# Optimization experiments

Measured on AMD Instinct MI355X. Metric: run time of the kernel, lower is better.

## Reference

```python
import jax, jax.numpy as jnp
import numpy as np

B, I, H = 65536, 256, 256

def setup_inputs() -> dict:
    key = jax.random.key(0)
    ks = jax.random.split(key, 7)
    stdv = 1.0 / np.sqrt(H)
    u = lambda k, shape: jax.random.uniform(k, shape, jnp.float32, -stdv, stdv)
    return {
        "x":  jax.random.normal(ks[0], (B, I), jnp.float32),
        "h":  jax.random.normal(ks[1], (B, H), jnp.float32),
        "c":  jax.random.normal(ks[2], (B, H), jnp.float32),
        "Wi": u(ks[3], (4, H, I)),   # stacked [W_ii, W_if, W_ig, W_io], torch layout [out,in]
        "Wh": u(ks[4], (4, H, H)),   # stacked [W_hi, W_hf, W_hg, W_ho]
        "bi": u(ks[5], (4, H)),
        "bh": u(ks[6], (4, H)),
    }

def reference(x, h, c, Wi, Wh, bi, bh):
    # Fused version of 8 separate Linears: two batched GEMMs + one elementwise pass.
    # gates[b, k, h] = x @ Wi[k].T + h_prev @ Wh[k].T + bi[k] + bh[k]
    gates = (jnp.einsum('bi,khi->bkh', x, Wi)
             + jnp.einsum('bj,khj->bkh', h, Wh)
             + bi[None] + bh[None])
    i = jax.nn.sigmoid(gates[:, 0])
    f = jax.nn.sigmoid(gates[:, 1])
    g = jnp.tanh(gates[:, 2])
    o = jax.nn.sigmoid(gates[:, 3])
    c_new = f * c + i * g
    h_new = o * jnp.tanh(c_new)
    return (h_new, c_new)
```

## Files before the change

kernel.cpp:

```cpp
#include <hip/hip_runtime.h>
#include <stdint.h>

#define B_DIM 65536
#define HOFF  16777216

typedef __attribute__((ext_vector_type(8))) short short8;
typedef __attribute__((ext_vector_type(8))) unsigned short ushort8_t;
typedef __attribute__((ext_vector_type(4))) float f32x4;

__device__ __forceinline__ unsigned short f2bf(float f) {
  unsigned int u = __builtin_bit_cast(unsigned int, f);
  u += 0x7FFFu + ((u >> 16) & 1u);
  return (unsigned short)(u >> 16);
}
__device__ __forceinline__ float sigf(float x) { return 1.0f / (1.0f + __expf(-x)); }
__device__ __forceinline__ float tanh_fast(float x) {
  float a = fabsf(x);
  float e = __expf(-2.0f * a);
  float t = (1.0f - e) / (1.0f + e);
  return x < 0.0f ? -t : t;
}

typedef const __attribute__((address_space(1))) unsigned int* as1p;
typedef __attribute__((address_space(3))) unsigned int* as3p;
__device__ __forceinline__ void llds16(const unsigned short* g, unsigned short* l) {
  __builtin_amdgcn_global_load_lds((as1p)g, (as3p)l, 16, 0, 0);
}

__global__ void prep_a(const float* __restrict__ x, const float* __restrict__ h,
                       ushort8_t* __restrict__ A8) {
  unsigned o = blockIdx.x * 256u + threadIdx.x;
  unsigned b = o >> 6, c8 = o & 63u;
  const float* src = (c8 < 32u) ? x + (size_t)b * 256u + c8 * 8u
                                : h + (size_t)b * 256u + (c8 - 32u) * 8u;
  float4 v0 = *(const float4*)src;
  float4 v1 = *(const float4*)(src + 4);
  ushort8_t p;
  p[0] = f2bf(v0.x); p[1] = f2bf(v0.y); p[2] = f2bf(v0.z); p[3] = f2bf(v0.w);
  p[4] = f2bf(v1.x); p[5] = f2bf(v1.y); p[6] = f2bf(v1.z); p[7] = f2bf(v1.w);
  A8[o] = p;
}

__global__ void prep_w(const float* __restrict__ Wi, const float* __restrict__ Wh,
                       ushort8_t* __restrict__ W8) {
  unsigned o = blockIdx.x * 256u + threadIdx.x;
  unsigned n = o >> 6, c8 = o & 63u;
  const float* src = (c8 < 32u) ? Wi + (size_t)n * 256u + c8 * 8u
                                : Wh + (size_t)n * 256u + (c8 - 32u) * 8u;
  float4 v0 = *(const float4*)src;
  float4 v1 = *(const float4*)(src + 4);
  ushort8_t p;
  p[0] = f2bf(v0.x); p[1] = f2bf(v0.y); p[2] = f2bf(v0.z); p[3] = f2bf(v0.w);
  p[4] = f2bf(v1.x); p[5] = f2bf(v1.y); p[6] = f2bf(v1.z); p[7] = f2bf(v1.w);
  W8[o] = p;
}

__global__ __launch_bounds__(256, 4) void lstm_gemm(
    const unsigned short* __restrict__ A,
    const unsigned short* __restrict__ W,
    const float* __restrict__ cprev,
    const float* __restrict__ bi, const float* __restrict__ bh,
    float* __restrict__ out) {
  __shared__ unsigned short sA[128 * 32];
  __shared__ unsigned short sB[128 * 32];

  const int t = threadIdx.x;
  const int wid = t >> 6, lane = t & 63;
  const int m = lane & 15, q = lane >> 4;
  const int b0 = (int)(blockIdx.x >> 3) * 128;
  const int h0 = (int)(blockIdx.x & 7) * 32;
  const int R = (wid >> 1) * 64, Cc = (wid & 1) * 64;
  const int hcol = h0 + ((Cc >> 6) << 4) + m;

  const int l4 = lane >> 2;
  const int sg0 = wid * 2, sg1 = wid * 2 + 1;
  const int r0 = sg0 * 16 + l4, r1 = sg1 * 16 + l4;
  const int ck = ((lane & 3) ^ ((l4 >> 1) & 3)) * 8;
  const unsigned aO0 = (unsigned)(b0 + r0) * 512u + (unsigned)ck;
  const unsigned aO1 = (unsigned)(b0 + r1) * 512u + (unsigned)ck;
  const int n0 = (((r0 >> 4) & 3) << 8) + h0 + (r0 & 15) + ((r0 >> 6) << 4);
  const int n1 = (((r1 >> 4) & 3) << 8) + h0 + (r1 & 15) + ((r1 >> 6) << 4);
  const unsigned wO0 = (unsigned)n0 * 512u + (unsigned)ck;
  const unsigned wO1 = (unsigned)n1 * 512u + (unsigned)ck;
  unsigned short* dA0 = &sA[sg0 * 512];
  unsigned short* dA1 = &sA[sg1 * 512];
  unsigned short* dB0 = &sB[sg0 * 512];
  unsigned short* dB1 = &sB[sg1 * 512];

  const int swz = (q ^ ((m >> 1) & 3)) * 8;

  f32x4 acc[4][4];
#pragma unroll
  for (int j = 0; j < 4; ++j) {
    float bv = bi[(j << 8) + hcol] + bh[(j << 8) + hcol];
    f32x4 z = {bv, bv, bv, bv};
#pragma unroll
    for (int i = 0; i < 4; ++i) acc[i][j] = z;
  }

  for (int kt = 0; kt < 16; ++kt) {
    const unsigned k0 = kt * 32u;
    llds16(A + aO0 + k0, dA0);
    llds16(A + aO1 + k0, dA1);
    llds16(W + wO0 + k0, dB0);
    llds16(W + wO1 + k0, dB1);
    __syncthreads();
    short8 av[4], bv[4];
#pragma unroll
    for (int i = 0; i < 4; ++i)
      av[i] = *(const short8*)&sA[(R + i * 16 + m) * 32 + swz];
#pragma unroll
    for (int j = 0; j < 4; ++j)
      bv[j] = *(const short8*)&sB[(Cc + j * 16 + m) * 32 + swz];
#pragma unroll
    for (int i = 0; i < 4; ++i)
#pragma unroll
      for (int j = 0; j < 4; ++j)
        acc[i][j] = __builtin_amdgcn_mfma_f32_16x16x32_bf16(av[i], bv[j], acc[i][j], 0, 0, 0);
    __syncthreads();
  }

  const float* cp = cprev + hcol;
  float* oh = out + hcol;
  float* oc = out + HOFF + hcol;
#pragma unroll
  for (int i = 0; i < 4; ++i) {
    const int br = b0 + R + i * 16 + (q << 2);
    float cv[4];
#pragma unroll
    for (int r = 0; r < 4; ++r) cv[r] = cp[(size_t)(br + r) << 8];
#pragma unroll
    for (int r = 0; r < 4; ++r) {
      float iv = sigf(acc[i][0][r]);
      float fv = sigf(acc[i][1][r]);
      float gv = tanh_fast(acc[i][2][r]);
      float ov = sigf(acc[i][3][r]);
      float cn = fv * cv[r] + iv * gv;
      oh[(size_t)(br + r) << 8] = ov * tanh_fast(cn);
      oc[(size_t)(br + r) << 8] = cn;
    }
  }
}

__global__ void lstm_naive(const float* __restrict__ x, const float* __restrict__ h,
                           const float* __restrict__ c,
                           const float* __restrict__ Wi, const float* __restrict__ Wh,
                           const float* __restrict__ bi, const float* __restrict__ bh,
                           float* __restrict__ out) {
  int gid = blockIdx.x * 256 + threadIdx.x;
  int b = gid >> 8, hh = gid & 255;
  float a0 = bi[hh] + bh[hh];
  float a1 = bi[256 + hh] + bh[256 + hh];
  float a2 = bi[512 + hh] + bh[512 + hh];
  float a3 = bi[768 + hh] + bh[768 + hh];
  const float* xr = x + (size_t)b * 256;
  const float* hr = h + (size_t)b * 256;
  const float* w0 = Wi + (size_t)hh * 256;
  const float* w1 = Wh + (size_t)hh * 256;
  for (int i = 0; i < 256; ++i) {
    float xv = xr[i];
    a0 += xv * w0[i]; a1 += xv * w0[65536 + i];
    a2 += xv * w0[131072 + i]; a3 += xv * w0[196608 + i];
  }
  for (int i = 0; i < 256; ++i) {
    float hv = hr[i];
    a0 += hv * w1[i]; a1 += hv * w1[65536 + i];
    a2 += hv * w1[131072 + i]; a3 += hv * w1[196608 + i];
  }
  float iv = sigf(a0), fv = sigf(a1), gv = tanh_fast(a2), ov = sigf(a3);
  float cn = fv * c[gid] + iv * gv;
  out[gid] = ov * tanh_fast(cn);
  out[HOFF + gid] = cn;
}

extern "C" void kernel_launch(void* const* d_in, const int* in_sizes, int n_in,
                              void* d_out, int out_size, void* d_ws, size_t ws_size,
                              hipStream_t stream) {
  const float* x  = (const float*)d_in[0];
  const float* h  = (const float*)d_in[1];
  const float* c  = (const float*)d_in[2];
  const float* Wi = (const float*)d_in[3];
  const float* Wh = (const float*)d_in[4];
  const float* bi = (const float*)d_in[5];
  const float* bh = (const float*)d_in[6];
  float* out = (float*)d_out;

  const size_t needA = (size_t)B_DIM * 512 * 2;
  const size_t needW = (size_t)1024 * 512 * 2;
  if (ws_size >= needA + needW) {
    ushort8_t* A8 = (ushort8_t*)d_ws;
    ushort8_t* W8 = (ushort8_t*)((char*)d_ws + needA);
    hipLaunchKernelGGL(prep_a, dim3(B_DIM * 64 / 256), dim3(256), 0, stream, x, h, A8);
    hipLaunchKernelGGL(prep_w, dim3(1024 * 64 / 256), dim3(256), 0, stream, Wi, Wh, W8);
    hipLaunchKernelGGL(lstm_gemm, dim3((B_DIM / 128) * 8), dim3(256), 0, stream,
                       (const unsigned short*)A8, (const unsigned short*)W8,
                       c, bi, bh, out);
  } else {
    hipLaunchKernelGGL(lstm_naive, dim3(B_DIM), dim3(256), 0, stream,
                       x, h, c, Wi, Wh, bi, bh, out);
  }
}
```

Baseline: 413.8 us.

## Widen K-step, remap blocks per XCD, stage epilogue stores through LDS

Doubles the K tile per iteration to 64 (two 32-wide LDS halves) so the loop has half as many barrier pairs. Remaps block IDs so that all blocks on one XCD share the same batch rows, improving L2 reuse of the A tile across the 8 h-column blocks. The epilogue now goes through LDS to emit coalesced float4 row stores instead of strided scalar stores, at the cost of extra barriers. LDS per block grows to 32 KB and launch bounds drop to 3 blocks per SM, which may reduce occupancy.

After: 360.3 us. -12.9%, faster.

```diff
diff --git a/kernel.cpp b/kernel.cpp
--- a/kernel.cpp
+++ b/kernel.cpp
@@ -55,20 +55,25 @@
   W8[o] = p;
 }
 
-__global__ __launch_bounds__(256, 4) void lstm_gemm(
+__global__ __launch_bounds__(256, 3) void lstm_gemm(
     const unsigned short* __restrict__ A,
     const unsigned short* __restrict__ W,
     const float* __restrict__ cprev,
     const float* __restrict__ bi, const float* __restrict__ bh,
     float* __restrict__ out) {
-  __shared__ unsigned short sA[128 * 32];
-  __shared__ unsigned short sB[128 * 32];
+  __shared__ __align__(16) char smem[32768];
+  unsigned short* sA = (unsigned short*)smem;
+  unsigned short* sB = (unsigned short*)(smem + 16384);
 
   const int t = threadIdx.x;
   const int wid = t >> 6, lane = t & 63;
   const int m = lane & 15, q = lane >> 4;
-  const int b0 = (int)(blockIdx.x >> 3) * 128;
-  const int h0 = (int)(blockIdx.x & 7) * 32;
+
+  const unsigned bid = blockIdx.x;
+  const unsigned xcd = bid & 7u, kk_ = bid >> 3;
+  const int b0 = (int)((xcd * 64u + (kk_ >> 3)) * 128u);
+  const int h0 = (int)((kk_ & 7u) * 32u);
+
   const int R = (wid >> 1) * 64, Cc = (wid & 1) * 64;
   const int hcol = h0 + ((Cc >> 6) << 4) + m;
 
@@ -82,10 +87,10 @@
   const int n1 = (((r1 >> 4) & 3) << 8) + h0 + (r1 & 15) + ((r1 >> 6) << 4);
   const unsigned wO0 = (unsigned)n0 * 512u + (unsigned)ck;
   const unsigned wO1 = (unsigned)n1 * 512u + (unsigned)ck;
-  unsigned short* dA0 = &sA[sg0 * 512];
-  unsigned short* dA1 = &sA[sg1 * 512];
-  unsigned short* dB0 = &sB[sg0 * 512];
-  unsigned short* dB1 = &sB[sg1 * 512];
+  unsigned short* dA0 = sA + sg0 * 512;
+  unsigned short* dA1 = sA + sg1 * 512;
+  unsigned short* dB0 = sB + sg0 * 512;
+  unsigned short* dB1 = sB + sg1 * 512;
 
   const int swz = (q ^ ((m >> 1) & 3)) * 8;
 
@@ -98,31 +103,50 @@
     for (int i = 0; i < 4; ++i) acc[i][j] = z;
   }
 
-  for (int kt = 0; kt < 16; ++kt) {
-    const unsigned k0 = kt * 32u;
+  for (int kt = 0; kt < 8; ++kt) {
+    const unsigned k0 = kt * 64u;
     llds16(A + aO0 + k0, dA0);
     llds16(A + aO1 + k0, dA1);
     llds16(W + wO0 + k0, dB0);
     llds16(W + wO1 + k0, dB1);
+    llds16(A + aO0 + k0 + 32u, dA0 + 4096);
+    llds16(A + aO1 + k0 + 32u, dA1 + 4096);
+    llds16(W + wO0 + k0 + 32u, dB0 + 4096);
+    llds16(W + wO1 + k0 + 32u, dB1 + 4096);
     __syncthreads();
-    short8 av[4], bv[4];
-#pragma unroll
-    for (int i = 0; i < 4; ++i)
-      av[i] = *(const short8*)&sA[(R + i * 16 + m) * 32 + swz];
-#pragma unroll
-    for (int j = 0; j < 4; ++j)
-      bv[j] = *(const short8*)&sB[(Cc + j * 16 + m) * 32 + swz];
-#pragma unroll
-    for (int i = 0; i < 4; ++i)
+    {
+      short8 av[4], bv[4];
+#pragma unroll
+      for (int i = 0; i < 4; ++i)
+        av[i] = *(const short8*)&sA[(R + i * 16 + m) * 32 + swz];
 #pragma unroll
       for (int j = 0; j < 4; ++j)
-        acc[i][j] = __builtin_amdgcn_mfma_f32_16x16x32_bf16(av[i], bv[j], acc[i][j], 0, 0, 0);
+        bv[j] = *(const short8*)&sB[(Cc + j * 16 + m) * 32 + swz];
+#pragma unroll
+      for (int i = 0; i < 4; ++i)
+#pragma unroll
+        for (int j = 0; j < 4; ++j)
+          acc[i][j] = __builtin_amdgcn_mfma_f32_16x16x32_bf16(av[i], bv[j], acc[i][j], 0, 0, 0);
+    }
+    {
+      short8 av[4], bv[4];
+#pragma unroll
+      for (int i = 0; i < 4; ++i)
+        av[i] = *(const short8*)&sA[4096 + (R + i * 16 + m) * 32 + swz];
+#pragma unroll
+      for (int j = 0; j < 4; ++j)
+        bv[j] = *(const short8*)&sB[4096 + (Cc + j * 16 + m) * 32 + swz];
+#pragma unroll
+      for (int i = 0; i < 4; ++i)
+#pragma unroll
+        for (int j = 0; j < 4; ++j)
+          acc[i][j] = __builtin_amdgcn_mfma_f32_16x16x32_bf16(av[i], bv[j], acc[i][j], 0, 0, 0);
+    }
     __syncthreads();
   }
 
   const float* cp = cprev + hcol;
-  float* oh = out + hcol;
-  float* oc = out + HOFF + hcol;
+  float hn[4][4], cn[4][4];
 #pragma unroll
   for (int i = 0; i < 4; ++i) {
     const int br = b0 + R + i * 16 + (q << 2);
@@ -135,10 +159,40 @@
       float fv = sigf(acc[i][1][r]);
       float gv = tanh_fast(acc[i][2][r]);
       float ov = sigf(acc[i][3][r]);
-      float cn = fv * cv[r] + iv * gv;
-      oh[(size_t)(br + r) << 8] = ov * tanh_fast(cn);
-      oc[(size_t)(br + r) << 8] = cn;
+      float c2 = fv * cv[r] + iv * gv;
+      cn[i][r] = c2;
+      hn[i][r] = ov * tanh_fast(c2);
     }
+  }
+
+  float* ep = (float*)smem;
+  const int ecol = ((Cc >> 6) << 4) + m;
+#pragma unroll
+  for (int i = 0; i < 4; ++i)
+#pragma unroll
+    for (int r = 0; r < 4; ++r)
+      ep[(R + i * 16 + (q << 2) + r) * 36 + ecol] = hn[i][r];
+  __syncthreads();
+#pragma unroll
+  for (int k = 0; k < 4; ++k) {
+    const int id = t + k * 256;
+    const int row = id >> 3, c4 = id & 7;
+    *(float4*)(out + ((size_t)(b0 + row) << 8) + h0 + c4 * 4) =
+        *(const float4*)&ep[row * 36 + c4 * 4];
+  }
+  __syncthreads();
+#pragma unroll
+  for (int i = 0; i < 4; ++i)
+#pragma unroll
+    for (int r = 0; r < 4; ++r)
+      ep[(R + i * 16 + (q << 2) + r) * 36 + ecol] = cn[i][r];
+  __syncthreads();
+#pragma unroll
+  for (int k = 0; k < 4; ++k) {
+    const int id = t + k * 256;
+    const int row = id >> 3, c4 = id & 7;
+    *(float4*)(out + HOFF + ((size_t)(b0 + row) << 8) + h0 + c4 * 4) =
+        *(const float4*)&ep[row * 36 + c4 * 4];
   }
 }
 
```

## Rewrite LSTM GEMM with 256x256 tiles, double-buffered LDS pipeline and staged epilogue

Applied to the files above, without the earlier changes.

The GEMM kernel moves to 512-thread blocks that each compute a 256-row by 256-gate-column tile (64 hidden columns across 4 gates). The K loop is double-buffered across a 128 KB LDS region with global_load_lds prefetches interleaved between MFMA phases, raised MFMA priority, and XCD-aware block-to-tile mapping. The epilogue stages h and c through LDS so the global stores become coalesced float4 writes. The goal is more operand reuse, memory latency hidden behind compute, and cheaper stores. The cost is heavy LDS use that allows only one block per CU, plus fragile manual vmcnt bookkeeping.

Measured after the change: 499.5 us. +20.7%, slower.

```diff
diff --git a/kernel.cpp b/kernel.cpp
--- a/kernel.cpp
+++ b/kernel.cpp
@@ -55,90 +55,190 @@
   W8[o] = p;
 }
 
-__global__ __launch_bounds__(256, 4) void lstm_gemm(
+__global__ __launch_bounds__(512, 2) void lstm_gemm(
     const unsigned short* __restrict__ A,
     const unsigned short* __restrict__ W,
     const float* __restrict__ cprev,
     const float* __restrict__ bi, const float* __restrict__ bh,
     float* __restrict__ out) {
-  __shared__ unsigned short sA[128 * 32];
-  __shared__ unsigned short sB[128 * 32];
+  __shared__ __align__(16) char smem[131072];
+  unsigned short* const sU = (unsigned short*)smem;
 
   const int t = threadIdx.x;
   const int wid = t >> 6, lane = t & 63;
   const int m = lane & 15, q = lane >> 4;
-  const int b0 = (int)(blockIdx.x >> 3) * 128;
-  const int h0 = (int)(blockIdx.x & 7) * 32;
-  const int R = (wid >> 1) * 64, Cc = (wid & 1) * 64;
-  const int hcol = h0 + ((Cc >> 6) << 4) + m;
-
-  const int l4 = lane >> 2;
-  const int sg0 = wid * 2, sg1 = wid * 2 + 1;
-  const int r0 = sg0 * 16 + l4, r1 = sg1 * 16 + l4;
-  const int ck = ((lane & 3) ^ ((l4 >> 1) & 3)) * 8;
-  const unsigned aO0 = (unsigned)(b0 + r0) * 512u + (unsigned)ck;
-  const unsigned aO1 = (unsigned)(b0 + r1) * 512u + (unsigned)ck;
-  const int n0 = (((r0 >> 4) & 3) << 8) + h0 + (r0 & 15) + ((r0 >> 6) << 4);
-  const int n1 = (((r1 >> 4) & 3) << 8) + h0 + (r1 & 15) + ((r1 >> 6) << 4);
-  const unsigned wO0 = (unsigned)n0 * 512u + (unsigned)ck;
-  const unsigned wO1 = (unsigned)n1 * 512u + (unsigned)ck;
-  unsigned short* dA0 = &sA[sg0 * 512];
-  unsigned short* dA1 = &sA[sg1 * 512];
-  unsigned short* dB0 = &sB[sg0 * 512];
-  unsigned short* dB1 = &sB[sg1 * 512];
-
-  const int swz = (q ^ ((m >> 1) & 3)) * 8;
-
-  f32x4 acc[4][4];
-#pragma unroll
-  for (int j = 0; j < 4; ++j) {
-    float bv = bi[(j << 8) + hcol] + bh[(j << 8) + hcol];
-    f32x4 z = {bv, bv, bv, bv};
-#pragma unroll
-    for (int i = 0; i < 4; ++i) acc[i][j] = z;
-  }
-
-  for (int kt = 0; kt < 16; ++kt) {
-    const unsigned k0 = kt * 32u;
-    llds16(A + aO0 + k0, dA0);
-    llds16(A + aO1 + k0, dA1);
-    llds16(W + wO0 + k0, dB0);
-    llds16(W + wO1 + k0, dB1);
-    __syncthreads();
-    short8 av[4], bv[4];
-#pragma unroll
-    for (int i = 0; i < 4; ++i)
-      av[i] = *(const short8*)&sA[(R + i * 16 + m) * 32 + swz];
-#pragma unroll
-    for (int j = 0; j < 4; ++j)
-      bv[j] = *(const short8*)&sB[(Cc + j * 16 + m) * 32 + swz];
-#pragma unroll
-    for (int i = 0; i < 4; ++i)
-#pragma unroll
-      for (int j = 0; j < 4; ++j)
-        acc[i][j] = __builtin_amdgcn_mfma_f32_16x16x32_bf16(av[i], bv[j], acc[i][j], 0, 0, 0);
-    __syncthreads();
-  }
-
-  const float* cp = cprev + hcol;
-  float* oh = out + hcol;
-  float* oc = out + HOFF + hcol;
-#pragma unroll
-  for (int i = 0; i < 4; ++i) {
-    const int br = b0 + R + i * 16 + (q << 2);
-    float cv[4];
-#pragma unroll
-    for (int r = 0; r < 4; ++r) cv[r] = cp[(size_t)(br + r) << 8];
+  const int wr = wid >> 2, wc = wid & 3;
+
+  const unsigned bid = blockIdx.x;
+  const unsigned xcd = bid & 7u, idx = bid >> 3;
+  const int b0 = (int)((xcd * 32u + (idx >> 2)) * 256u);
+  const int h0 = (int)((idx & 3u) * 64u);
+
+  const int l3 = lane >> 3;
+  const unsigned ckg = (unsigned)((((lane & 7) ^ l3)) * 8);
+  unsigned aSrc[2][2], bSrc[2][2];
+#pragma unroll
+  for (int hh = 0; hh < 2; ++hh)
+#pragma unroll
+    for (int j = 0; j < 2; ++j) {
+      const int s = 2 * wid + j;
+      aSrc[hh][j] = (unsigned)(b0 + hh * 128 + s * 8 + l3) * 512u + ckg;
+      const int n = (2 * hh + ((s >> 1) & 1)) * 256 + h0 +
+                    ((s >> 2) & 3) * 16 + (s & 1) * 8 + l3;
+      bSrc[hh][j] = (unsigned)n * 512u + ckg;
+    }
+  const int dstSeg = 2 * wid * 512;
+
+  const int aBase = wr * 4096 + m * 64;
+  const int bBase = wc * 2048 + m * 64;
+  const int c0 = ((q) ^ (m & 7)) * 8;
+  const int c1 = ((4 + q) ^ (m & 7)) * 8;
+
+  const int hcol = h0 + wc * 16 + m;
+
+  f32x4 acc[8][4];
+#pragma unroll
+  for (int g = 0; g < 4; ++g) {
+    float bvv = bi[(g << 8) + hcol] + bh[(g << 8) + hcol];
+    f32x4 z = {bvv, bvv, bvv, bvv};
+#pragma unroll
+    for (int mi = 0; mi < 8; ++mi) acc[mi][g] = z;
+  }
+
+  short8 av[4][2], bv[2][2];
+  float cv[8][4];
+
+  auto stA = [&](int buf, int ha, int kt) {
+    unsigned short* d = sU + buf * 32768 + ha * 8192 + dstSeg;
+    const unsigned ko = (unsigned)kt * 64u;
+    llds16(A + aSrc[ha][0] + ko, d);
+    llds16(A + aSrc[ha][1] + ko, d + 512);
+  };
+  auto stB = [&](int buf, int hb, int kt) {
+    unsigned short* d = sU + buf * 32768 + 16384 + hb * 8192 + dstSeg;
+    const unsigned ko = (unsigned)kt * 64u;
+    llds16(W + bSrc[hb][0] + ko, d);
+    llds16(W + bSrc[hb][1] + ko, d + 512);
+  };
+  auto rdA = [&](int buf, int qa) {
+    const unsigned short* p = sU + buf * 32768 + qa * 8192 + aBase;
+#pragma unroll
+    for (int fi = 0; fi < 4; ++fi) {
+      av[fi][0] = *(const short8*)(p + fi * 1024 + c0);
+      av[fi][1] = *(const short8*)(p + fi * 1024 + c1);
+    }
+  };
+  auto rdB = [&](int buf, int qb) {
+    const unsigned short* p = sU + buf * 32768 + 16384 + qb * 8192 + bBase;
+#pragma unroll
+    for (int f = 0; f < 2; ++f) {
+      bv[f][0] = *(const short8*)(p + f * 1024 + c0);
+      bv[f][1] = *(const short8*)(p + f * 1024 + c1);
+    }
+  };
+  auto mm = [&](int mi0, int nj0) {
+    __builtin_amdgcn_s_setprio(1);
+#pragma unroll
+    for (int fi = 0; fi < 4; ++fi)
+#pragma unroll
+      for (int f = 0; f < 2; ++f)
+#pragma unroll
+        for (int kk = 0; kk < 2; ++kk)
+          acc[mi0 + fi][nj0 + f] = __builtin_amdgcn_mfma_f32_16x16x32_bf16(
+              av[fi][kk], bv[f][kk], acc[mi0 + fi][nj0 + f], 0, 0, 0);
+    __builtin_amdgcn_s_setprio(0);
+  };
+  auto bar = [&] {
+    __builtin_amdgcn_s_barrier();
+    __builtin_amdgcn_sched_barrier(0);
+  };
+
+  stA(0, 0, 0); stB(0, 0, 0); stA(0, 1, 0); stB(0, 1, 0);
+  stA(1, 0, 1); stB(1, 0, 1);
+  asm volatile("s_waitcnt vmcnt(4)" ::: "memory");
+  bar();
+
+#pragma unroll 2
+  for (int kt = 0; kt < 8; ++kt) {
+    const int cur = kt & 1;
+    rdA(cur, 0); rdB(cur, 0);
+    if (kt < 7) stA(cur ^ 1, 1, kt + 1);
+    if (kt == 7) {
+#pragma unroll
+      for (int mi = 0; mi < 8; ++mi) {
+        const int br = b0 + (mi >> 2) * 128 + wr * 64 + (mi & 3) * 16 + (q << 2);
+#pragma unroll
+        for (int r = 0; r < 4; ++r)
+          cv[mi][r] = cprev[(size_t)(br + r) * 256 + hcol];
+      }
+    }
+    bar();
+    mm(0, 0);
+    bar();
+    rdB(cur, 1);
+    if (kt < 7) stB(cur ^ 1, 1, kt + 1);
+    bar();
+    mm(0, 2);
+    bar();
+    rdA(cur, 1); rdB(cur, 0);
+    if (kt < 6) stA(cur, 0, kt + 2);
+    bar();
+    mm(4, 0);
+    bar();
+    rdB(cur, 1);
+    if (kt < 6) stB(cur, 0, kt + 2);
+    bar();
+    mm(4, 2);
+    if (kt < 6) asm volatile("s_waitcnt vmcnt(4)" ::: "memory");
+    else if (kt == 6) asm volatile("s_waitcnt vmcnt(0)" ::: "memory");
+    bar();
+  }
+
+  asm volatile("s_waitcnt vmcnt(0) lgkmcnt(0)" ::: "memory");
+  bar();
+
+  float* ep = (float*)smem;
+  float cn[8][4];
+#pragma unroll
+  for (int mi = 0; mi < 8; ++mi) {
+    const int row = (mi >> 2) * 128 + wr * 64 + (mi & 3) * 16 + (q << 2);
 #pragma unroll
     for (int r = 0; r < 4; ++r) {
-      float iv = sigf(acc[i][0][r]);
-      float fv = sigf(acc[i][1][r]);
-      float gv = tanh_fast(acc[i][2][r]);
-      float ov = sigf(acc[i][3][r]);
-      float cn = fv * cv[r] + iv * gv;
-      oh[(size_t)(br + r) << 8] = ov * tanh_fast(cn);
-      oc[(size_t)(br + r) << 8] = cn;
-    }
+      float iv = sigf(acc[mi][0][r]);
+      float fv = sigf(acc[mi][1][r]);
+      float gv = tanh_fast(acc[mi][2][r]);
+      float ov = sigf(acc[mi][3][r]);
+      float c2 = fv * cv[mi][r] + iv * gv;
+      cn[mi][r] = c2;
+      ep[(row + r) * 68 + wc * 16 + m] = ov * tanh_fast(c2);
+    }
+  }
+  asm volatile("s_waitcnt lgkmcnt(0)" ::: "memory");
+  bar();
+#pragma unroll
+  for (int k = 0; k < 8; ++k) {
+    const int id = t + k * 512;
+    const int row = id >> 4, c4 = id & 15;
+    *(float4*)(out + ((size_t)(b0 + row) << 8) + h0 + c4 * 4) =
+        *(const float4*)&ep[row * 68 + c4 * 4];
+  }
+  asm volatile("s_waitcnt lgkmcnt(0)" ::: "memory");
+  bar();
+#pragma unroll
+  for (int mi = 0; mi < 8; ++mi) {
+    const int row = (mi >> 2) * 128 + wr * 64 + (mi & 3) * 16 + (q << 2);
+#pragma unroll
+    for (int r = 0; r < 4; ++r)
+      ep[(row + r) * 68 + wc * 16 + m] = cn[mi][r];
+  }
+  asm volatile("s_waitcnt lgkmcnt(0)" ::: "memory");
+  bar();
+#pragma unroll
+  for (int k = 0; k < 8; ++k) {
+    const int id = t + k * 512;
+    const int row = id >> 4, c4 = id & 15;
+    *(float4*)(out + HOFF + ((size_t)(b0 + row) << 8) + h0 + c4 * 4) =
+        *(const float4*)&ep[row * 68 + c4 * 4];
   }
 }
 
@@ -192,7 +292,7 @@
     ushort8_t* W8 = (ushort8_t*)((char*)d_ws + needA);
     hipLaunchKernelGGL(prep_a, dim3(B_DIM * 64 / 256), dim3(256), 0, stream, x, h, A8);
     hipLaunchKernelGGL(prep_w, dim3(1024 * 64 / 256), dim3(256), 0, stream, Wi, Wh, W8);
-    hipLaunchKernelGGL(lstm_gemm, dim3((B_DIM / 128) * 8), dim3(256), 0, stream,
+    hipLaunchKernelGGL(lstm_gemm, dim3((B_DIM / 256) * 4), dim3(512), 0, stream,
                        (const unsigned short*)A8, (const unsigned short*)W8,
                        c, bi, bh, out);
   } else {
```
